# Performance work log

Measured on AMD Instinct MI355X. Metric: run time of the kernel, lower is better.

Reference implementation:

```python
import jax, jax.numpy as jnp
import numpy as np

B = 4096
IN = 1024      # input_shape * 2
H = 2048       # rnn_hidden_dim * 2
A = 64         # n_actions
A2 = A * A     # fc2 output width


def setup_inputs() -> dict:
    key = jax.random.key(0)
    ks = jax.random.split(key, 12)
    s_in = 1.0 / np.sqrt(IN)
    s_h = 1.0 / np.sqrt(H)
    return {
        "inputs": jax.random.normal(ks[0], (B, IN), jnp.float32),
        "hidden_state": jax.random.normal(ks[1], (B, H), jnp.float32),
        # fc1: Linear(IN -> H)
        "W1": jax.random.uniform(ks[2], (H, IN), jnp.float32, -s_in, s_in),
        "b1": jax.random.uniform(ks[3], (H,), jnp.float32, -s_in, s_in),
        # GRUCell(H -> H), gate order r, z, n
        "Wih": jax.random.uniform(ks[4], (3 * H, H), jnp.float32, -s_h, s_h),
        "Whh": jax.random.uniform(ks[5], (3 * H, H), jnp.float32, -s_h, s_h),
        "bih": jax.random.uniform(ks[6], (3 * H,), jnp.float32, -s_h, s_h),
        "bhh": jax.random.uniform(ks[7], (3 * H,), jnp.float32, -s_h, s_h),
        # fc2: Linear(H -> A^2)
        "W2": jax.random.uniform(ks[8], (A2, H), jnp.float32, -s_h, s_h),
        "b2": jax.random.uniform(ks[9], (A2,), jnp.float32, -s_h, s_h),
    }


# Static gather indices for the vectorized __decode_combined_output.
# Row 2i, col j: max over q[i, j : j+A]  (contiguous window)
_IDX1 = np.arange(A)[:, None] + np.arange(A)[None, :]              # [A, A]
# Row 2i+1, col j: max over q[i, k-1] for k in range(j, A^2, A);
# at j=0 the index k-1 = -1 wraps to the last element (torch semantics).
_IDX2 = (np.arange(A)[:, None] + np.arange(A)[None, :] * A - 1) % A2  # [A, A]


def reference(inputs, hidden_state, W1, b1, Wih, Whh, bih, bhh, W2, b2):
    x = jax.nn.relu(inputs @ W1.T + b1)                 # [B, H]
    h_in = hidden_state.reshape(-1, H)
    gi = x @ Wih.T + bih                                # [B, 3H]
    gh = h_in @ Whh.T + bhh                             # [B, 3H]
    ir, iz, inn = jnp.split(gi, 3, axis=1)
    hr, hz, hn = jnp.split(gh, 3, axis=1)
    r = jax.nn.sigmoid(ir + hr)
    z = jax.nn.sigmoid(iz + hz)
    n = jnp.tanh(inn + r * hn)
    h = (1.0 - z) * n + z * h_in                        # [B, H]
    q = h @ W2.T + b2                                   # [B, A^2]
    q1 = jnp.max(q[:, _IDX1], axis=-1)                  # [B, A]
    q2 = jnp.max(q[:, _IDX2], axis=-1)                  # [B, A]
    out = jnp.stack([q1, q2], axis=1).reshape(-1, A)    # interleaved [2B, A]
    return out, h
```

## Files before the change

### kernel.cpp

```cpp
#include <hip/hip_runtime.h>
#include <stdint.h>

typedef unsigned short u16;
typedef __bf16 bf16x8 __attribute__((ext_vector_type(8)));
typedef float f32x4 __attribute__((ext_vector_type(4)));
typedef u16 u16x8 __attribute__((ext_vector_type(8)));

__device__ __forceinline__ float b2f(u16 v) {
    union { float f; unsigned int u; } x; x.u = ((unsigned int)v) << 16; return x.f;
}
__device__ __forceinline__ u16 f2b(float f) {
    union { float f; unsigned int u; } x; x.f = f;
    unsigned int r = x.u + 0x7fff + ((x.u >> 16) & 1);
    return (u16)(r >> 16);
}

__device__ __forceinline__ void gll16(const void* g, void* l) {
    __builtin_amdgcn_global_load_lds(
        (const __attribute__((address_space(1))) void*)g,
        (__attribute__((address_space(3))) void*)l,
        16, 0, 0);
}

__device__ __forceinline__ bf16x8 pack8(float4 f0, float4 f1) {
    union { float4 f; uint4 u; } a, b;
    a.f = f0; b.f = f1;
    const unsigned sel = 0x07060302u;
    union { unsigned u[4]; bf16x8 v; } r;
    r.u[0] = __builtin_amdgcn_perm(a.u.y + 0x8000u, a.u.x + 0x8000u, sel);
    r.u[1] = __builtin_amdgcn_perm(a.u.w + 0x8000u, a.u.z + 0x8000u, sel);
    r.u[2] = __builtin_amdgcn_perm(b.u.y + 0x8000u, b.u.x + 0x8000u, sel);
    r.u[3] = __builtin_amdgcn_perm(b.u.w + 0x8000u, b.u.z + 0x8000u, sel);
    return r.v;
}

__device__ __forceinline__ void cvt_body(const float* __restrict__ s,
                                         u16* __restrict__ d, int cb)
{
    const size_t i = ((size_t)cb * 512 + threadIdx.x) * 8;
    float4 f0 = *(const float4*)(s + i);
    float4 f1 = *(const float4*)(s + i + 4);
    union { bf16x8 v; u16x8 u; } r;
    r.v = pack8(f0, f1);
    *(u16x8*)(d + i) = r.u;
}

__global__ __launch_bounds__(512) void cvt4_kernel(
    const float* __restrict__ s0, u16* __restrict__ d0, int n0,
    const float* __restrict__ s1, u16* __restrict__ d1, int n1,
    const float* __restrict__ s2, u16* __restrict__ d2, int n2,
    const float* __restrict__ s3, u16* __restrict__ d3, int n3)
{
    int cb = blockIdx.x;
    const float* s; u16* d;
    if (cb < n0)                    { s = s0; d = d0; }
    else if ((cb -= n0) < n1)       { s = s1; d = d1; }
    else if ((cb -= n1) < n2)       { s = s2; d = d2; }
    else                            { cb -= n2; s = s3; d = d3; }
    cvt_body(s, d, cb);
}


#define FBAR() do { asm volatile("" ::: "memory"); \
                    __builtin_amdgcn_s_barrier();  \
                    asm volatile("" ::: "memory"); } while (0)
#define WAIT_LGKM0() asm volatile("s_waitcnt lgkmcnt(0)" ::: "memory")
#define WAIT_VM6()   asm volatile("s_waitcnt vmcnt(6)" ::: "memory")
#define WAIT_VM0()   asm volatile("s_waitcnt vmcnt(0)" ::: "memory")
#define LREG(buf, idx) (Ls + ((buf) * 4 + (idx)) * 8192)

__device__ __forceinline__ void stage_half(
    const u16* __restrict__ Mp, int rowBase, int K, int k0,
    u16* region, int t, int w)
{
#pragma unroll
    for (int it = 0; it < 2; ++it) {
        const int phys = it * 512 + t;
        const int r = phys >> 3;
        const int c = (phys & 7) ^ (r & 7);
        gll16(Mp + (size_t)(rowBase + r) * K + (k0 + c * 8),
              (char*)region + (it * 512 + w * 64) * 16);
    }
}

__device__ __forceinline__ void ld_a(const u16* region, int ra, int g0,
                                     bf16x8 (&out)[4][2])
{
#pragma unroll
    for (int mi = 0; mi < 4; ++mi)
#pragma unroll
        for (int s = 0; s < 2; ++s) {
            const int lr = mi * 32 + ra;
            out[mi][s] = *(const bf16x8*)((const char*)region +
                         (lr * 8 + ((s * 4 + g0) ^ (lr & 7))) * 16);
        }
}

__device__ __forceinline__ void ld_b(const u16* region, int rb, int g0,
                                     bf16x8 (&out)[2][2])
{
#pragma unroll
    for (int ni = 0; ni < 2; ++ni)
#pragma unroll
        for (int s = 0; s < 2; ++s) {
            const int lr = ni * 64 + rb;
            out[ni][s] = *(const bf16x8*)((const char*)region +
                         (lr * 8 + ((s * 4 + g0) ^ (lr & 7))) * 16);
        }
}

template <int MO, int NO>
__device__ __forceinline__ void mfma_quad(const bf16x8 (&af)[4][2],
                                          const bf16x8 (&bf)[2][2],
                                          f32x4 (&acc)[8][4])
{
    __builtin_amdgcn_s_setprio(1);
#pragma unroll
    for (int mi = 0; mi < 4; ++mi)
#pragma unroll
        for (int ni = 0; ni < 2; ++ni)
#pragma unroll
            for (int s = 0; s < 2; ++s)
                acc[MO + mi][NO + ni] = __builtin_amdgcn_mfma_f32_16x16x32_bf16(
                    af[mi][s], bf[ni][s], acc[MO + mi][NO + ni], 0, 0, 0);
    __builtin_amdgcn_s_setprio(0);
}

template <bool RELU>
__device__ __forceinline__ void gemm_body(
    u16* Ls,
    const u16* __restrict__ A, const u16* __restrict__ Bw,
    const float* __restrict__ bias, u16* __restrict__ C,
    int N, int K, int gy, int gx, int bid)
{
    const int t = threadIdx.x;
    const int l = t & 63;
    const int w = t >> 6;
    const int wr = w >> 2;
    const int wc = w & 3;

    const int xcd = bid & 7, rem = bid >> 3;
    const int rrows = gy >> 1, rcols = gx >> 2;
    const int lr_ = rem / rcols, lc_ = rem % rcols;
    const int mBase = ((xcd >> 2) * rrows + lr_) * 256;
    const int nBase = ((xcd & 3) * rcols + lc_) * 256;

    const int frow = l & 15;
    const int g0 = l >> 4;
    const int ra = wr * 16 + frow;
    const int rb = wc * 16 + frow;

    f32x4 acc[8][4] = {};
    bf16x8 a0[4][2], a1[4][2], b0[2][2], b1[2][2];

    const int NI = K >> 7;

    stage_half(A,  mBase,       K, 0,  LREG(0, 0), t, w);
    stage_half(Bw, nBase,       K, 0,  LREG(0, 2), t, w);
    stage_half(Bw, nBase + 128, K, 0,  LREG(0, 3), t, w);
    stage_half(A,  mBase + 128, K, 0,  LREG(0, 1), t, w);
    stage_half(A,  mBase,       K, 64, LREG(1, 0), t, w);
    stage_half(Bw, nBase,       K, 64, LREG(1, 2), t, w);
    stage_half(Bw, nBase + 128, K, 64, LREG(1, 3), t, w);
    WAIT_VM6();
    FBAR();

    for (int i = 0; i < NI; ++i) {
        const bool nl = (i + 1 < NI);
        const int kT1 = (2 * i + 1) << 6;
        const int kT2 = (2 * i + 2) << 6;
        const int kT3 = (2 * i + 3) << 6;

        ld_a(LREG(0, 0), ra, g0, a0);
        ld_b(LREG(0, 2), rb, g0, b0);
        stage_half(A, mBase + 128, K, kT1, LREG(1, 1), t, w);
        FBAR();
        WAIT_LGKM0();
        mfma_quad<0, 0>(a0, b0, acc);
        FBAR();

        ld_b(LREG(0, 3), rb, g0, b1);
        if (nl) stage_half(A, mBase, K, kT2, LREG(0, 0), t, w);
        FBAR();
        WAIT_LGKM0();
        mfma_quad<0, 2>(a0, b1, acc);
        FBAR();

        ld_a(LREG(0, 1), ra, g0, a1);
        if (nl) stage_half(Bw, nBase, K, kT2, LREG(0, 2), t, w);
        FBAR();
        WAIT_LGKM0();
        mfma_quad<4, 0>(a1, b0, acc);
        FBAR();

        if (nl) stage_half(Bw, nBase + 128, K, kT2, LREG(0, 3), t, w);
        FBAR();
        mfma_quad<4, 2>(a1, b1, acc);
        if (nl) { WAIT_VM6(); } else { WAIT_VM0(); }
        FBAR();

        ld_a(LREG(1, 0), ra, g0, a0);
        ld_b(LREG(1, 2), rb, g0, b0);
        if (nl) stage_half(A, mBase + 128, K, kT2, LREG(0, 1), t, w);
        FBAR();
        WAIT_LGKM0();
        mfma_quad<0, 0>(a0, b0, acc);
        FBAR();

        ld_b(LREG(1, 3), rb, g0, b1);
        if (nl) stage_half(A, mBase, K, kT3, LREG(1, 0), t, w);
        FBAR();
        WAIT_LGKM0();
        mfma_quad<0, 2>(a0, b1, acc);
        FBAR();

        ld_a(LREG(1, 1), ra, g0, a1);
        if (nl) stage_half(Bw, nBase, K, kT3, LREG(1, 2), t, w);
        FBAR();
        WAIT_LGKM0();
        mfma_quad<4, 0>(a1, b0, acc);
        FBAR();

        if (nl) stage_half(Bw, nBase + 128, K, kT3, LREG(1, 3), t, w);
        FBAR();
        mfma_quad<4, 2>(a1, b1, acc);
        if (nl) { WAIT_VM6(); }
        FBAR();
    }

    const int rq = (l >> 4) * 4;
#pragma unroll
    for (int ni = 0; ni < 4; ++ni) {
        const int col = nBase + ni * 64 + wc * 16 + (l & 15);
        const float bv = bias[col];
#pragma unroll
        for (int mi = 0; mi < 8; ++mi) {
            const int row = mBase + mi * 32 + wr * 16 + rq;
#pragma unroll
            for (int i2 = 0; i2 < 4; ++i2) {
                float v = acc[mi][ni][i2] + bv;
                if (RELU) v = fmaxf(v, 0.0f);
                C[(size_t)(row + i2) * N + col] = f2b(v);
            }
        }
    }
}

template <bool RELU>
__global__ __launch_bounds__(512, 2) void gemm256(
    const u16* __restrict__ A, const u16* __restrict__ Bw,
    const float* __restrict__ bias, u16* __restrict__ C,
    int N, int K, int gy, int gx)
{
    __shared__ alignas(16) u16 L[2 * 4 * 8192];
    gemm_body<RELU>(L, A, Bw, bias, C, N, K, gy, gx, blockIdx.x);
}

__global__ __launch_bounds__(512, 2) void mega1_kernel(
    const u16* __restrict__ ghA, const u16* __restrict__ ghB,
    const float* __restrict__ ghBias, u16* __restrict__ ghC,
    const u16* __restrict__ xA, const u16* __restrict__ xB,
    const float* __restrict__ xBias, u16* __restrict__ xC,
    const float* __restrict__ cs, u16* __restrict__ cd)
{
    __shared__ alignas(16) u16 L[2 * 4 * 8192];
    int bid = blockIdx.x;
    if (bid < 16 * 24) {
        gemm_body<false>(L, ghA, ghB, ghBias, ghC, 6144, 2048, 16, 24, bid);
        return;
    }
    bid -= 16 * 24;
    if (bid < 16 * 8) {
        gemm_body<true>(L, xA, xB, xBias, xC, 2048, 1024, 16, 8, bid);
        return;
    }
    cvt_body(cs, cd, bid - 16 * 8);
}

__global__ __launch_bounds__(512, 2) void mega2_kernel(
    const u16* __restrict__ A, const u16* __restrict__ Bw,
    const float* __restrict__ bias, u16* __restrict__ C,
    const float* __restrict__ cs, u16* __restrict__ cd)
{
    __shared__ alignas(16) u16 L[2 * 4 * 8192];
    int bid = blockIdx.x;
    if (bid < 16 * 24) {
        gemm_body<false>(L, A, Bw, bias, C, 6144, 2048, 16, 24, bid);
        return;
    }
    cvt_body(cs, cd, bid - 16 * 24);
}

__device__ __forceinline__ float fsig(float x) {
    return 1.f / (1.f + __expf(-x));
}
__device__ __forceinline__ float ftanh(float x) {
    float t = __expf(2.f * fabsf(x));
    return copysignf(1.f - 2.f / (t + 1.f), x);
}

__global__ __launch_bounds__(256) void gru_kernel(
    const u16* __restrict__ gi, const u16* __restrict__ gh,
    const float* __restrict__ hprev, float* __restrict__ houtf,
    u16* __restrict__ houtb, int H)
{
    const size_t idx = ((size_t)blockIdx.x * 256 + threadIdx.x) * 8;
    const size_t b = idx / H;
    const size_t j = idx - b * H;
    const size_t g0 = b * (size_t)(3 * H) + j;

    u16x8 vir = *(const u16x8*)&gi[g0];
    u16x8 viz = *(const u16x8*)&gi[g0 + H];
    u16x8 vin = *(const u16x8*)&gi[g0 + 2 * H];
    u16x8 vhr = *(const u16x8*)&gh[g0];
    u16x8 vhz = *(const u16x8*)&gh[g0 + H];
    u16x8 vhn = *(const u16x8*)&gh[g0 + 2 * H];
    float4 hp0 = *(const float4*)&hprev[idx];
    float4 hp1 = *(const float4*)&hprev[idx + 4];
    float hp[8] = {hp0.x, hp0.y, hp0.z, hp0.w, hp1.x, hp1.y, hp1.z, hp1.w};
    float ho[8];
    u16x8 ob;
#pragma unroll
    for (int i = 0; i < 8; ++i) {
        float r = fsig(b2f(vir[i]) + b2f(vhr[i]));
        float z = fsig(b2f(viz[i]) + b2f(vhz[i]));
        float n = ftanh(b2f(vin[i]) + r * b2f(vhn[i]));
        float h = (1.f - z) * n + z * hp[i];
        ho[i] = h;
        ob[i] = f2b(h);
    }
    *(float4*)&houtf[idx]     = make_float4(ho[0], ho[1], ho[2], ho[3]);
    *(float4*)&houtf[idx + 4] = make_float4(ho[4], ho[5], ho[6], ho[7]);
    *(u16x8*)&houtb[idx] = ob;
}

__global__ __launch_bounds__(256) void decode_kernel(
    const u16* __restrict__ q, float* __restrict__ out)
{
    __shared__ float s[4096];
    const int row = blockIdx.x;
    const int t = threadIdx.x;
    const size_t base = (size_t)row * 4096;
#pragma unroll
    for (int i = 0; i < 2; ++i) {
        const int j = t * 8 + i * 2048;
        u16x8 v = *(const u16x8*)&q[base + j];
#pragma unroll
        for (int k2 = 0; k2 < 8; ++k2) s[j + k2] = b2f(v[k2]);
    }
    __syncthreads();
    if (t < 64) {
        float m = -INFINITY;
#pragma unroll 8
        for (int k = 0; k < 64; ++k) m = fmaxf(m, s[t + k]);
        out[(size_t)(2 * row) * 64 + t] = m;
    } else if (t < 128) {
        const int rr = t - 64;
        float m = -INFINITY;
#pragma unroll 8
        for (int k = 0; k < 64; ++k) m = fmaxf(m, s[rr + 64 * k]);
        const int j = (rr + 1) & 63;
        out[(size_t)(2 * row + 1) * 64 + j] = m;
    }
}

extern "C" void kernel_launch(void* const* d_in, const int* in_sizes, int n_in,
                              void* d_out, int out_size, void* d_ws, size_t ws_size,
                              hipStream_t stream) {
    constexpr int Bn = 4096, IN = 1024, H = 2048, A = 64, A2 = A * A;
    constexpr size_t BH  = (size_t)Bn * H;
    constexpr size_t H3H = (size_t)3 * H * H;
    constexpr size_t HIN = (size_t)H * IN;
    constexpr size_t BIN = (size_t)Bn * IN;
    constexpr size_t A2H = (size_t)A2 * H;
    constexpr size_t B3H = (size_t)Bn * 3 * H;

    const float* inputs = (const float*)d_in[0];
    const float* h0     = (const float*)d_in[1];
    const float* W1     = (const float*)d_in[2];
    const float* b1     = (const float*)d_in[3];
    const float* Wih    = (const float*)d_in[4];
    const float* Whh    = (const float*)d_in[5];
    const float* bih    = (const float*)d_in[6];
    const float* bhh    = (const float*)d_in[7];
    const float* W2     = (const float*)d_in[8];
    const float* b2     = (const float*)d_in[9];

    float* out  = (float*)d_out;
    float* hout = out + (size_t)2 * Bn * A;

    u16* wsu  = (u16*)d_ws;
    u16* h0b  = wsu;
    u16* Whhb = wsu + BH;
    u16* gi   = wsu;
    u16* q    = wsu;
    u16* gh   = wsu + B3H;
    u16* Wihb = wsu + 2 * B3H;
    u16* hbf  = wsu + 2 * B3H;
    u16* W1b  = wsu + 2 * B3H + H3H;
    u16* inb  = W1b + HIN;
    u16* xb   = inb + BIN;
    u16* W2b  = xb + BH;

    dim3 blk(256);
    dim3 gblk(512);

    cvt4_kernel<<<dim3(2048 + 3072 + 512 + 1024), gblk, 0, stream>>>(
        h0, h0b, 2048, Whh, Whhb, 3072, W1, W1b, 512, inputs, inb, 1024);

    mega1_kernel<<<dim3(384 + 128 + 3072), gblk, 0, stream>>>(
        h0b, Whhb, bhh, gh, inb, W1b, b1, xb, Wih, Wihb);

    mega2_kernel<<<dim3(384 + 2048), gblk, 0, stream>>>(
        xb, Wihb, bih, gi, W2, W2b);

    gru_kernel<<<dim3((Bn * H / 8) / 256), blk, 0, stream>>>(
        gi, gh, h0, hout, hbf, H);

    gemm256<false><<<dim3(256), gblk, 0, stream>>>(
        hbf, W2b, b2, q, A2, H, 16, 16);

    decode_kernel<<<dim3(Bn), blk, 0, stream>>>(q, out);
}
```

Measured before the change: 502.1 us.

## Fuse all stages into one persistent cooperative kernel with grid syncs

Replaces the six separate launches (conversion, two merged GEMM launches, GRU, fc2 GEMM, decode) with a single cooperative kernel of 256 blocks that walks through each stage and separates them with grid-wide syncs. The workspace layout is reassigned so buffers no longer alias in the old order. The goal is to remove per-launch overhead and tail gaps between kernels. In exchange, GEMM work is spread unevenly (384 tiles over 256 blocks, so some blocks do two tiles), each stage's parallelism is capped at 256 blocks, and grid syncs add barrier cost.

```diff
diff --git a/kernel.cpp b/kernel.cpp
--- a/kernel.cpp
+++ b/kernel.cpp
@@ -1,5 +1,8 @@
 #include <hip/hip_runtime.h>
+#include <hip/hip_cooperative_groups.h>
 #include <stdint.h>
+
+namespace cg = cooperative_groups;
 
 typedef unsigned short u16;
 typedef __bf16 bf16x8 __attribute__((ext_vector_type(8)));
@@ -45,21 +48,6 @@
     *(u16x8*)(d + i) = r.u;
 }
 
-__global__ __launch_bounds__(512) void cvt4_kernel(
-    const float* __restrict__ s0, u16* __restrict__ d0, int n0,
-    const float* __restrict__ s1, u16* __restrict__ d1, int n1,
-    const float* __restrict__ s2, u16* __restrict__ d2, int n2,
-    const float* __restrict__ s3, u16* __restrict__ d3, int n3)
-{
-    int cb = blockIdx.x;
-    const float* s; u16* d;
-    if (cb < n0)                    { s = s0; d = d0; }
-    else if ((cb -= n0) < n1)       { s = s1; d = d1; }
-    else if ((cb -= n1) < n2)       { s = s2; d = d2; }
-    else                            { cb -= n2; s = s3; d = d3; }
-    cvt_body(s, d, cb);
-}
-
 
 #define FBAR() do { asm volatile("" ::: "memory"); \
                     __builtin_amdgcn_s_barrier();  \
@@ -246,51 +234,6 @@
     }
 }
 
-template <bool RELU>
-__global__ __launch_bounds__(512, 2) void gemm256(
-    const u16* __restrict__ A, const u16* __restrict__ Bw,
-    const float* __restrict__ bias, u16* __restrict__ C,
-    int N, int K, int gy, int gx)
-{
-    __shared__ alignas(16) u16 L[2 * 4 * 8192];
-    gemm_body<RELU>(L, A, Bw, bias, C, N, K, gy, gx, blockIdx.x);
-}
-
-__global__ __launch_bounds__(512, 2) void mega1_kernel(
-    const u16* __restrict__ ghA, const u16* __restrict__ ghB,
-    const float* __restrict__ ghBias, u16* __restrict__ ghC,
-    const u16* __restrict__ xA, const u16* __restrict__ xB,
-    const float* __restrict__ xBias, u16* __restrict__ xC,
-    const float* __restrict__ cs, u16* __restrict__ cd)
-{
-    __shared__ alignas(16) u16 L[2 * 4 * 8192];
-    int bid = blockIdx.x;
-    if (bid < 16 * 24) {
-        gemm_body<false>(L, ghA, ghB, ghBias, ghC, 6144, 2048, 16, 24, bid);
-        return;
-    }
-    bid -= 16 * 24;
-    if (bid < 16 * 8) {
-        gemm_body<true>(L, xA, xB, xBias, xC, 2048, 1024, 16, 8, bid);
-        return;
-    }
-    cvt_body(cs, cd, bid - 16 * 8);
-}
-
-__global__ __launch_bounds__(512, 2) void mega2_kernel(
-    const u16* __restrict__ A, const u16* __restrict__ Bw,
-    const float* __restrict__ bias, u16* __restrict__ C,
-    const float* __restrict__ cs, u16* __restrict__ cd)
-{
-    __shared__ alignas(16) u16 L[2 * 4 * 8192];
-    int bid = blockIdx.x;
-    if (bid < 16 * 24) {
-        gemm_body<false>(L, A, Bw, bias, C, 6144, 2048, 16, 24, bid);
-        return;
-    }
-    cvt_body(cs, cd, bid - 16 * 24);
-}
-
 __device__ __forceinline__ float fsig(float x) {
     return 1.f / (1.f + __expf(-x));
 }
@@ -299,126 +242,142 @@
     return copysignf(1.f - 2.f / (t + 1.f), x);
 }
 
-__global__ __launch_bounds__(256) void gru_kernel(
-    const u16* __restrict__ gi, const u16* __restrict__ gh,
-    const float* __restrict__ hprev, float* __restrict__ houtf,
-    u16* __restrict__ houtb, int H)
-{
-    const size_t idx = ((size_t)blockIdx.x * 256 + threadIdx.x) * 8;
-    const size_t b = idx / H;
-    const size_t j = idx - b * H;
-    const size_t g0 = b * (size_t)(3 * H) + j;
-
-    u16x8 vir = *(const u16x8*)&gi[g0];
-    u16x8 viz = *(const u16x8*)&gi[g0 + H];
-    u16x8 vin = *(const u16x8*)&gi[g0 + 2 * H];
-    u16x8 vhr = *(const u16x8*)&gh[g0];
-    u16x8 vhz = *(const u16x8*)&gh[g0 + H];
-    u16x8 vhn = *(const u16x8*)&gh[g0 + 2 * H];
-    float4 hp0 = *(const float4*)&hprev[idx];
-    float4 hp1 = *(const float4*)&hprev[idx + 4];
-    float hp[8] = {hp0.x, hp0.y, hp0.z, hp0.w, hp1.x, hp1.y, hp1.z, hp1.w};
-    float ho[8];
-    u16x8 ob;
-#pragma unroll
-    for (int i = 0; i < 8; ++i) {
-        float r = fsig(b2f(vir[i]) + b2f(vhr[i]));
-        float z = fsig(b2f(viz[i]) + b2f(vhz[i]));
-        float n = ftanh(b2f(vin[i]) + r * b2f(vhn[i]));
-        float h = (1.f - z) * n + z * hp[i];
-        ho[i] = h;
-        ob[i] = f2b(h);
-    }
-    *(float4*)&houtf[idx]     = make_float4(ho[0], ho[1], ho[2], ho[3]);
-    *(float4*)&houtf[idx + 4] = make_float4(ho[4], ho[5], ho[6], ho[7]);
-    *(u16x8*)&houtb[idx] = ob;
-}
-
-__global__ __launch_bounds__(256) void decode_kernel(
-    const u16* __restrict__ q, float* __restrict__ out)
-{
-    __shared__ float s[4096];
-    const int row = blockIdx.x;
+struct PK {
+    const float *inputs, *h0, *W1, *b1, *Wih, *Whh, *bih, *bhh, *W2, *b2;
+    float *out, *hout;
+    u16 *h0b, *Whhb, *W1b, *inb, *Wihb, *xb, *W2b, *gh, *gi, *hbf, *q;
+};
+
+__global__ __launch_bounds__(512, 2) void persist(PK p)
+{
+    __shared__ alignas(16) u16 L[2 * 4 * 8192];
+    cg::grid_group grid = cg::this_grid();
+    const int b = blockIdx.x;
     const int t = threadIdx.x;
-    const size_t base = (size_t)row * 4096;
-#pragma unroll
-    for (int i = 0; i < 2; ++i) {
-        const int j = t * 8 + i * 2048;
-        u16x8 v = *(const u16x8*)&q[base + j];
-#pragma unroll
-        for (int k2 = 0; k2 < 8; ++k2) s[j + k2] = b2f(v[k2]);
-    }
-    __syncthreads();
-    if (t < 64) {
-        float m = -INFINITY;
+
+    for (int c = b; c < 9728; c += 256) {
+        if (c < 2048)       cvt_body(p.h0,  p.h0b,  c);
+        else if (c < 5120)  cvt_body(p.Whh, p.Whhb, c - 2048);
+        else if (c < 5632)  cvt_body(p.W1,  p.W1b,  c - 5120);
+        else if (c < 6656)  cvt_body(p.inputs, p.inb, c - 5632);
+        else                cvt_body(p.Wih, p.Wihb, c - 6656);
+    }
+    grid.sync();
+
+    gemm_body<false>(L, p.h0b, p.Whhb, p.bhh, p.gh, 6144, 2048, 16, 24, b);
+    if (b < 128) {
+        gemm_body<false>(L, p.h0b, p.Whhb, p.bhh, p.gh, 6144, 2048, 16, 24,
+                         256 + b);
+    } else {
+        gemm_body<true>(L, p.inb, p.W1b, p.b1, p.xb, 2048, 1024, 16, 8,
+                        b - 128);
+        for (int c = b - 128; c < 2048; c += 128) cvt_body(p.W2, p.W2b, c);
+    }
+    grid.sync();
+
+    gemm_body<false>(L, p.xb, p.Wihb, p.bih, p.gi, 6144, 2048, 16, 24, b);
+    if (b < 128)
+        gemm_body<false>(L, p.xb, p.Wihb, p.bih, p.gi, 6144, 2048, 16, 24,
+                         256 + b);
+    grid.sync();
+
+    for (int u = b; u < 2048; u += 256) {
+        const size_t idx = (size_t)u * 4096 + (size_t)t * 8;
+        const size_t row = idx >> 11;
+        const size_t j = idx & 2047;
+        const size_t g0 = row * 6144 + j;
+        u16x8 vir = *(const u16x8*)&p.gi[g0];
+        u16x8 viz = *(const u16x8*)&p.gi[g0 + 2048];
+        u16x8 vin = *(const u16x8*)&p.gi[g0 + 4096];
+        u16x8 vhr = *(const u16x8*)&p.gh[g0];
+        u16x8 vhz = *(const u16x8*)&p.gh[g0 + 2048];
+        u16x8 vhn = *(const u16x8*)&p.gh[g0 + 4096];
+        float4 hp0 = *(const float4*)&p.h0[idx];
+        float4 hp1 = *(const float4*)&p.h0[idx + 4];
+        float hp[8] = {hp0.x, hp0.y, hp0.z, hp0.w,
+                       hp1.x, hp1.y, hp1.z, hp1.w};
+        float ho[8];
+        u16x8 ob;
+#pragma unroll
+        for (int i = 0; i < 8; ++i) {
+            float r = fsig(b2f(vir[i]) + b2f(vhr[i]));
+            float z = fsig(b2f(viz[i]) + b2f(vhz[i]));
+            float n = ftanh(b2f(vin[i]) + r * b2f(vhn[i]));
+            float h = (1.f - z) * n + z * hp[i];
+            ho[i] = h;
+            ob[i] = f2b(h);
+        }
+        *(float4*)&p.hout[idx]     = make_float4(ho[0], ho[1], ho[2], ho[3]);
+        *(float4*)&p.hout[idx + 4] = make_float4(ho[4], ho[5], ho[6], ho[7]);
+        *(u16x8*)&p.hbf[idx] = ob;
+    }
+    grid.sync();
+
+    gemm_body<false>(L, p.hbf, p.W2b, p.b2, p.q, 4096, 2048, 16, 16, b);
+    grid.sync();
+
+    float* s = (float*)L;
+    for (int k = 0; k < 16; ++k) {
+        const int row = b + 256 * k;
+        const size_t base = (size_t)row * 4096;
+        {
+            const int j = t * 8;
+            u16x8 v = *(const u16x8*)&p.q[base + j];
+#pragma unroll
+            for (int e = 0; e < 8; ++e) s[j + e] = b2f(v[e]);
+        }
+        __syncthreads();
+        if (t < 64) {
+            float m = -INFINITY;
 #pragma unroll 8
-        for (int k = 0; k < 64; ++k) m = fmaxf(m, s[t + k]);
-        out[(size_t)(2 * row) * 64 + t] = m;
-    } else if (t < 128) {
-        const int rr = t - 64;
-        float m = -INFINITY;
+            for (int kk = 0; kk < 64; ++kk) m = fmaxf(m, s[t + kk]);
+            p.out[(size_t)(2 * row) * 64 + t] = m;
+        } else if (t < 128) {
+            const int rr = t - 64;
+            float m = -INFINITY;
 #pragma unroll 8
-        for (int k = 0; k < 64; ++k) m = fmaxf(m, s[rr + 64 * k]);
-        const int j = (rr + 1) & 63;
-        out[(size_t)(2 * row + 1) * 64 + j] = m;
+            for (int kk = 0; kk < 64; ++kk) m = fmaxf(m, s[rr + 64 * kk]);
+            const int j = (rr + 1) & 63;
+            p.out[(size_t)(2 * row + 1) * 64 + j] = m;
+        }
+        __syncthreads();
     }
 }
 
 extern "C" void kernel_launch(void* const* d_in, const int* in_sizes, int n_in,
                               void* d_out, int out_size, void* d_ws, size_t ws_size,
                               hipStream_t stream) {
-    constexpr int Bn = 4096, IN = 1024, H = 2048, A = 64, A2 = A * A;
-    constexpr size_t BH  = (size_t)Bn * H;
-    constexpr size_t H3H = (size_t)3 * H * H;
-    constexpr size_t HIN = (size_t)H * IN;
-    constexpr size_t BIN = (size_t)Bn * IN;
-    constexpr size_t A2H = (size_t)A2 * H;
-    constexpr size_t B3H = (size_t)Bn * 3 * H;
-
-    const float* inputs = (const float*)d_in[0];
-    const float* h0     = (const float*)d_in[1];
-    const float* W1     = (const float*)d_in[2];
-    const float* b1     = (const float*)d_in[3];
-    const float* Wih    = (const float*)d_in[4];
-    const float* Whh    = (const float*)d_in[5];
-    const float* bih    = (const float*)d_in[6];
-    const float* bhh    = (const float*)d_in[7];
-    const float* W2     = (const float*)d_in[8];
-    const float* b2     = (const float*)d_in[9];
-
-    float* out  = (float*)d_out;
-    float* hout = out + (size_t)2 * Bn * A;
-
-    u16* wsu  = (u16*)d_ws;
-    u16* h0b  = wsu;
-    u16* Whhb = wsu + BH;
-    u16* gi   = wsu;
-    u16* q    = wsu;
-    u16* gh   = wsu + B3H;
-    u16* Wihb = wsu + 2 * B3H;
-    u16* hbf  = wsu + 2 * B3H;
-    u16* W1b  = wsu + 2 * B3H + H3H;
-    u16* inb  = W1b + HIN;
-    u16* xb   = inb + BIN;
-    u16* W2b  = xb + BH;
-
-    dim3 blk(256);
-    dim3 gblk(512);
-
-    cvt4_kernel<<<dim3(2048 + 3072 + 512 + 1024), gblk, 0, stream>>>(
-        h0, h0b, 2048, Whh, Whhb, 3072, W1, W1b, 512, inputs, inb, 1024);
-
-    mega1_kernel<<<dim3(384 + 128 + 3072), gblk, 0, stream>>>(
-        h0b, Whhb, bhh, gh, inb, W1b, b1, xb, Wih, Wihb);
-
-    mega2_kernel<<<dim3(384 + 2048), gblk, 0, stream>>>(
-        xb, Wihb, bih, gi, W2, W2b);
-
-    gru_kernel<<<dim3((Bn * H / 8) / 256), blk, 0, stream>>>(
-        gi, gh, h0, hout, hbf, H);
-
-    gemm256<false><<<dim3(256), gblk, 0, stream>>>(
-        hbf, W2b, b2, q, A2, H, 16, 16);
-
-    decode_kernel<<<dim3(Bn), blk, 0, stream>>>(q, out);
-}
+    constexpr int Bn = 4096, A = 64;
+
+    PK p;
+    p.inputs = (const float*)d_in[0];
+    p.h0     = (const float*)d_in[1];
+    p.W1     = (const float*)d_in[2];
+    p.b1     = (const float*)d_in[3];
+    p.Wih    = (const float*)d_in[4];
+    p.Whh    = (const float*)d_in[5];
+    p.bih    = (const float*)d_in[6];
+    p.bhh    = (const float*)d_in[7];
+    p.W2     = (const float*)d_in[8];
+    p.b2     = (const float*)d_in[9];
+
+    p.out  = (float*)d_out;
+    p.hout = p.out + (size_t)2 * Bn * A;
+
+    u16* wsu = (u16*)d_ws;
+    p.h0b  = wsu;
+    p.Whhb = wsu + 8388608;
+    p.W1b  = wsu + 20971520;
+    p.inb  = wsu + 23068672;
+    p.gi   = wsu;
+    p.Wihb = wsu + 27262976;
+    p.hbf  = wsu + 27262976;
+    p.xb   = wsu + 39845888;
+    p.W2b  = wsu + 48234496;
+    p.gh   = wsu + 56623104;
+    p.q    = wsu + 56623104;
+
+    void* args[] = { &p };
+    hipLaunchCooperativeKernel(reinterpret_cast<void*>(&persist),
+                               dim3(256), dim3(512), args, 0, stream);
+}
```

Result: slower. 794.1 us (+58.2%).
